# Kernel optimization log

Hardware: AMD Instinct MI355X
Metric: run time of the kernel (lower is better)

Reference implementation:

```python
import jax, jax.numpy as jnp
import numpy as np

N, E, H, ED = 10000, 160000, 512, 16
EPS = 1e-5
EDGE_SCALE = 0.1

def _ln(x, g, b):
    mu = jnp.mean(x, axis=-1, keepdims=True)
    var = jnp.mean(jnp.square(x - mu), axis=-1, keepdims=True)
    return (x - mu) * jax.lax.rsqrt(var + EPS) * g + b

def setup_inputs() -> dict:
    key = jax.random.key(0)
    ks = jax.random.split(key, 16)
    def w(k, i, o):
        return jax.random.normal(k, (i, o), jnp.float32) * (1.0 / np.sqrt(i))
    return {
        "h": jax.random.normal(ks[0], (N, H), jnp.float32),
        "edge_attr": jax.random.normal(ks[1], (E, ED), jnp.float32),
        "msg_w1": w(ks[2], H + ED, H), "msg_b1": jnp.zeros((H,), jnp.float32),
        "msg_w2": w(ks[3], H, H),      "msg_b2": jnp.zeros((H,), jnp.float32),
        "upd_w1": w(ks[4], 2 * H, H),  "upd_b1": jnp.zeros((H,), jnp.float32),
        "upd_w2": w(ks[5], H, H),      "upd_b2": jnp.zeros((H,), jnp.float32),
        "norm_g": jnp.ones((H,), jnp.float32), "norm_b": jnp.zeros((H,), jnp.float32),
        "em_w1": w(ks[6], 2 * H + ED, ED), "em_b1": jnp.zeros((ED,), jnp.float32),
        "em_w2": w(ks[7], ED, ED),         "em_b2": jnp.zeros((ED,), jnp.float32),
        "eg_w": w(ks[8], 2 * H + ED, 1),   "eg_b": jnp.zeros((1,), jnp.float32),
        "en_g": jnp.ones((ED,), jnp.float32), "en_b": jnp.zeros((ED,), jnp.float32),
        "edge_index": jax.random.randint(ks[9], (2, E), 0, N, jnp.int32),
    }

def reference(h, edge_attr, msg_w1, msg_b1, msg_w2, msg_b2,
              upd_w1, upd_b1, upd_w2, upd_b2, norm_g, norm_b,
              em_w1, em_b1, em_w2, em_b2, eg_w, eg_b, en_g, en_b,
              edge_index):
    src, dst = edge_index[0], edge_index[1]
    hs = h[src]                      # (E, H)
    hd = h[dst]                      # (E, H)
    # edge update with gating + scaled residual (eval: keep mask == 1)
    z = jnp.concatenate([hs, hd, edge_attr], axis=-1)   # (E, 2H+ED)
    gate = jax.nn.sigmoid(z @ eg_w + eg_b)               # (E, 1)
    delta = jax.nn.gelu(z @ em_w1 + em_b1, approximate=False) @ em_w2 + em_b2
    e_new = _ln(edge_attr + EDGE_SCALE * gate * delta, en_g, en_b)
    # message computation + scatter-add aggregation
    zm = jnp.concatenate([hs, e_new], axis=-1)           # (E, H+ED)
    m = jax.nn.gelu(zm @ msg_w1 + msg_b1, approximate=False) @ msg_w2 + msg_b2
    agg = jax.ops.segment_sum(m, dst, num_segments=h.shape[0])  # (N, H)
    # node update + residual + LayerNorm
    zu = jnp.concatenate([h, agg], axis=-1)              # (N, 2H)
    h2 = jax.nn.gelu(zu @ upd_w1 + upd_b1, approximate=False) @ upd_w2 + upd_b2
    h_out = _ln(h + h2, norm_g, norm_b)
    return (h_out, e_new)
```

## Files before the change

kernel.cpp:

```cpp
#include <hip/hip_runtime.h>

#define N_NODES 10000
#define N_EDGES 160000
#define HD 512
#define EDD 16

typedef unsigned short u16;
typedef __attribute__((ext_vector_type(8))) short bf16x8;
typedef __attribute__((ext_vector_type(4))) float f32x4;
typedef unsigned int u32;

__device__ __forceinline__ float bf2f(u16 u){
  unsigned int x = ((unsigned int)u) << 16;
  return __builtin_bit_cast(float, x);
}
__device__ __forceinline__ u16 f2bf(float f){
  unsigned int x = __builtin_bit_cast(unsigned int, f);
  unsigned int r = (x + 0x7fffu + ((x >> 16) & 1u)) >> 16;
  return (u16)r;
}
__device__ __forceinline__ float ldx(const void* p, long long i, int f32){
  return f32 ? ((const float*)p)[i] : bf2f(((const u16*)p)[i]);
}
__device__ __forceinline__ void stx(void* p, long long i, int f32, float v){
  if (f32) ((float*)p)[i] = v; else ((u16*)p)[i] = f2bf(v);
}
__device__ __forceinline__ float gelu_f(float x){
  float c = x * x;
  float a = x * (1.5957691216f + 0.0713548162f * c);
  float e = __expf(-a);
  return x * __builtin_amdgcn_rcpf(1.0f + e);
}
__device__ __forceinline__ f32x4 mfma16(bf16x8 a, bf16x8 b, f32x4 c){
  return __builtin_amdgcn_mfma_f32_16x16x32_bf16(a, b, c, 0, 0, 0);
}
__device__ __forceinline__ int swz8(int row, int slot){
  return (slot ^ ((row >> 1) & 3)) * 8;
}
__device__ __forceinline__ bf16x8 ld8(const void* p, long long i, int f32){
  if (!f32) return *(const bf16x8*)((const u16*)p + i);
  const float* q = (const float*)p + i;
  float4 a = *(const float4*)q, b = *(const float4*)(q + 4);
  u16 t[8] = { f2bf(a.x), f2bf(a.y), f2bf(a.z), f2bf(a.w),
               f2bf(b.x), f2bf(b.y), f2bf(b.z), f2bf(b.w) };
  return *(const bf16x8*)t;
}
__device__ __forceinline__ void stage8(const void* src, long long idx, int f32, u16* dst){
  bf16x8 v = ld8(src, idx, f32);
  *(bf16x8*)dst = v;
}

__device__ __forceinline__ int probe_rand(const void* p, int l){
  const u16* q = (const u16*)p;
  float mx = 0.f;
  #pragma unroll
  for (int i = 0; i < 4; ++i) mx = fmaxf(mx, fabsf(bf2f(q[l * 4 + i])));
  #pragma unroll
  for (int m = 1; m < 64; m <<= 1) mx = fmaxf(mx, __shfl_xor(mx, m, 64));
  return (mx > 1e3f) ? 1 : 0;
}
__global__ __launch_bounds__(64) void kprobe(
    const void* h, const void* ea, const void* mw1, const void* mw2,
    const void* uw1, const void* uw2, const void* ew1, const void* ew2,
    const void* egw, const void* ng, const void* eng, int* F)
{
  const int l = threadIdx.x;
  int f0 = probe_rand(h, l),   f1 = probe_rand(ea, l),  f2 = probe_rand(mw1, l);
  int f3 = probe_rand(mw2, l), f4 = probe_rand(uw1, l), f5 = probe_rand(uw2, l);
  int f6 = probe_rand(ew1, l), f7 = probe_rand(ew2, l), f8 = probe_rand(egw, l);
  if (l == 0){
    F[0] = f0; F[1] = f1; F[2] = f2; F[3] = f3; F[4] = f4; F[5] = f5;
    F[6] = f6; F[7] = f7; F[8] = f8;
    F[9]  = (((const u16*)ng)[0]  == 0) ? 1 : 0;
    F[10] = (((const u16*)eng)[0] == 0) ? 1 : 0;
    F[11] = f0;
  }
}

__global__ void kfill(u16* __restrict__ out, long long n, float val){
  long long i = (long long)blockIdx.x * 256 + threadIdx.x;
  if (i < n) out[i] = f2bf(val);
}

__global__ __launch_bounds__(256) void kprep(
    const void* __restrict__ h, const void* __restrict__ mw1,
    const void* __restrict__ mw2, const void* __restrict__ ew1,
    const void* __restrict__ egw, const int* __restrict__ F,
    u16* __restrict__ hB, u16* __restrict__ W1T, u16* __restrict__ W2T,
    u16* __restrict__ WceT)
{
  const int b = blockIdx.x, tid = threadIdx.x;
  if (b < 2500){
    const long long i = ((long long)b * 256 + tid) * 8;
    if (i < (long long)N_NODES * HD)
      *(bf16x8*)(hB + i) = ld8(h, i, F[0]);
  } else if (b < 3588){
    const int i = (b - 2500) * 256 + tid;
    const int n = i / 544, k = i - n * 544;
    u16 v = 0;
    if (k < 528) v = f2bf(ldx(mw1, (long long)k * 512 + n, F[2]));
    W1T[i] = v;
  } else if (b < 4612){
    const int i = (b - 3588) * 256 + tid;
    const int n = i >> 9, k = i & 511;
    W2T[i] = f2bf(ldx(mw2, (long long)k * 512 + n, F[3]));
  } else {
    const int i = (b - 4612) * 256 + tid;
    const int c = i >> 9, k = i & 511;
    float v = 0.f;
    if (c < 16)       v = ldx(ew1, (long long)k * 16 + c, F[6]);
    else if (c < 32)  v = ldx(ew1, (long long)(512 + k) * 16 + (c - 16), F[6]);
    else if (c == 32) v = ldx(egw, k, F[8]);
    else if (c == 33) v = ldx(egw, 512 + k, F[8]);
    WceT[i] = f2bf(v);
  }
}

__global__ __launch_bounds__(256) void kprep2(
    const void* __restrict__ uw1, const void* __restrict__ uw2,
    const int* __restrict__ F, u16* __restrict__ WU1T, u16* __restrict__ WU2T)
{
  const int b = blockIdx.x, tid = threadIdx.x;
  if (b < 2048){
    const int i = b * 256 + tid;
    const int n = i >> 10, k = i & 1023;
    WU1T[i] = f2bf(ldx(uw1, (long long)k * 512 + n, F[4]));
  } else {
    const int i = (b - 2048) * 256 + tid;
    const int n = i >> 9, k = i & 511;
    WU2T[i] = f2bf(ldx(uw2, (long long)k * 512 + n, F[5]));
  }
}

__global__ void kdeg(const int* __restrict__ dst, int* __restrict__ deg){
  int e = blockIdx.x * 256 + threadIdx.x;
  if (e < N_EDGES) atomicAdd(&deg[dst[e]], 1);
}

__global__ __launch_bounds__(256) void kscan(const int* __restrict__ deg,
                                             int* __restrict__ start){
  __shared__ int ls[256];
  const int t = threadIdx.x;
  const int base = t * 40;
  int s = 0;
  for (int i = 0; i < 40; ++i){ int idx = base + i; if (idx < N_NODES) s += deg[idx]; }
  ls[t] = s; __syncthreads();
  for (int off = 1; off < 256; off <<= 1){
    int v = (t >= off) ? ls[t - off] : 0;
    __syncthreads();
    ls[t] += v;
    __syncthreads();
  }
  int run = (t == 0) ? 0 : ls[t - 1];
  for (int i = 0; i < 40; ++i){
    int idx = base + i;
    if (idx < N_NODES){ start[idx] = run; run += deg[idx]; }
  }
}

__global__ void kscatter(const int* __restrict__ srcI, const int* __restrict__ dstI,
                         const int* __restrict__ start, int* __restrict__ cursor,
                         int* __restrict__ sSrc, int* __restrict__ sDst,
                         int* __restrict__ sIdx){
  int e = blockIdx.x * 256 + threadIdx.x;
  if (e < N_EDGES){
    int d = dstI[e];
    int p = start[d] + atomicAdd(&cursor[d], 1);
    sSrc[p] = srcI[e]; sDst[p] = d; sIdx[p] = e;
  }
}

__global__ __launch_bounds__(256, 4) void kpreP(
    const u16* __restrict__ hB, const u16* __restrict__ W1T,
    const void* __restrict__ msg_b1, const int* __restrict__ F,
    u16* __restrict__ P)
{
  __shared__ u16 As[128 * 32];
  __shared__ u16 Bs[64 * 32];
  const int tid = threadIdx.x;
  const int fw = F[2];
  const int row0 = blockIdx.x * 128, n0 = blockIdx.y * 64;
  f32x4 acc[2][4];
  f32x4 z4 = {0.f, 0.f, 0.f, 0.f};
  #pragma unroll
  for (int i = 0; i < 2; ++i)
    #pragma unroll
    for (int j = 0; j < 4; ++j) acc[i][j] = z4;
  const int w = tid >> 6, l = tid & 63;
  const int lm = l & 15, lk = l >> 4;
  const int nB = tid >> 2, kqB = tid & 3;
  for (int kt = 0; kt < 16; ++kt){
    const int kk = kt * 32;
    #pragma unroll
    for (int i = 0; i < 2; ++i){
      int t = tid + i * 256;
      int m = t >> 2, kq = t & 3;
      int gr = row0 + m; if (gr > N_NODES - 1) gr = N_NODES - 1;
      *(uint4*)&As[m * 32 + swz8(m, kq)] = *(const uint4*)(hB + (size_t)gr * HD + kk + kq * 8);
    }
    *(uint4*)&Bs[nB * 32 + swz8(nB, kqB)] =
        *(const uint4*)(W1T + (size_t)(n0 + nB) * 544 + kk + kqB * 8);
    __syncthreads();
    bf16x8 af[2], bfv[4];
    #pragma unroll
    for (int i = 0; i < 2; ++i){
      const int R = w * 32 + i * 16 + lm;
      af[i] = *(const bf16x8*)&As[R * 32 + swz8(R, lk)];
    }
    #pragma unroll
    for (int j = 0; j < 4; ++j){
      const int R = j * 16 + lm;
      bfv[j] = *(const bf16x8*)&Bs[R * 32 + swz8(R, lk)];
    }
    #pragma unroll
    for (int i = 0; i < 2; ++i)
      #pragma unroll
      for (int j = 0; j < 4; ++j)
        acc[i][j] = mfma16(af[i], bfv[j], acc[i][j]);
    __syncthreads();
  }
  #pragma unroll
  for (int j = 0; j < 4; ++j){
    const int col = n0 + j * 16 + lm;
    const float bias = ldx(msg_b1, col, fw);
    #pragma unroll
    for (int i = 0; i < 2; ++i){
      const int rb = row0 + w * 32 + i * 16 + lk * 4;
      #pragma unroll
      for (int r = 0; r < 4; ++r){
        int gr = rb + r;
        if (gr < N_NODES)
          P[(size_t)gr * HD + col] = f2bf(acc[i][j][r] + bias);
      }
    }
  }
}

__global__ __launch_bounds__(256) void kpreE(
    const u16* __restrict__ hB, const u16* __restrict__ WceT,
    u16* __restrict__ PE)
{
  __shared__ u16 As[128 * 32];
  __shared__ u16 Bs[48 * 32];
  const int tid = threadIdx.x;
  const int row0 = blockIdx.x * 128;
  f32x4 acc[2][3];
  f32x4 z4 = {0.f, 0.f, 0.f, 0.f};
  #pragma unroll
  for (int i = 0; i < 2; ++i)
    #pragma unroll
    for (int j = 0; j < 3; ++j) acc[i][j] = z4;
  const int w = tid >> 6, l = tid & 63;
  const int lm = l & 15, lk = l >> 4;
  for (int kt = 0; kt < 16; ++kt){
    const int kk = kt * 32;
    #pragma unroll
    for (int i = 0; i < 2; ++i){
      int t = tid + i * 256;
      int m = t >> 2, kq = t & 3;
      int gr = row0 + m; if (gr > N_NODES - 1) gr = N_NODES - 1;
      *(uint4*)&As[m * 32 + swz8(m, kq)] = *(const uint4*)(hB + (size_t)gr * HD + kk + kq * 8);
    }
    if (tid < 192){
      int c = tid >> 2, kq = tid & 3;
      *(uint4*)&Bs[c * 32 + swz8(c, kq)] =
          *(const uint4*)(WceT + (size_t)c * 512 + kk + kq * 8);
    }
    __syncthreads();
    bf16x8 af[2], bfv[3];
    #pragma unroll
    for (int i = 0; i < 2; ++i){
      const int R = w * 32 + i * 16 + lm;
      af[i] = *(const bf16x8*)&As[R * 32 + swz8(R, lk)];
    }
    #pragma unroll
    for (int j = 0; j < 3; ++j){
      const int R = j * 16 + lm;
      bfv[j] = *(const bf16x8*)&Bs[R * 32 + swz8(R, lk)];
    }
    #pragma unroll
    for (int i = 0; i < 2; ++i)
      #pragma unroll
      for (int j = 0; j < 3; ++j)
        acc[i][j] = mfma16(af[i], bfv[j], acc[i][j]);
    __syncthreads();
  }
  #pragma unroll
  for (int j = 0; j < 3; ++j){
    const int col = j * 16 + lm;
    #pragma unroll
    for (int i = 0; i < 2; ++i){
      const int rb = row0 + w * 32 + i * 16 + lk * 4;
      #pragma unroll
      for (int r = 0; r < 4; ++r){
        int gr = rb + r;
        if (gr < N_NODES)
          PE[(size_t)gr * 48 + col] = f2bf(acc[i][j][r]);
      }
    }
  }
}

__global__ __launch_bounds__(256) void kedge2(
    const void* __restrict__ ea, const u16* __restrict__ PE,
    const void* __restrict__ em_w1, const void* __restrict__ em_w2,
    const void* __restrict__ em_b1, const void* __restrict__ em_b2,
    const void* __restrict__ eg_w, const void* __restrict__ eg_b,
    const void* __restrict__ en_g, const void* __restrict__ en_b,
    const int* __restrict__ F,
    const int* __restrict__ srcI, const int* __restrict__ dstI,
    void* __restrict__ dout)
{
  __shared__ float wt[16][17];
  __shared__ float w2s[256];
  __shared__ float egt[16], b1e[16], b2s[16], gns[16], bns[16];
  __shared__ float egb_s;
  const int tid = threadIdx.x;
  const int fea = F[1], fem1 = F[6], fem2 = F[7], feg = F[8];
  const int fen = F[10], fo = F[11];
  { int k = tid >> 4, j = tid & 15;
    wt[k][j] = ldx(em_w1, (long long)(1024 + k) * 16 + j, fem1); }
  w2s[tid] = ldx(em_w2, tid, fem2);
  if (tid < 16){
    egt[tid] = ldx(eg_w, 1024 + tid, feg);
    b1e[tid] = ldx(em_b1, tid, fem1);
    b2s[tid] = ldx(em_b2, tid, fem2);
    gns[tid] = ldx(en_g, tid, fen);
    bns[tid] = ldx(en_b, tid, fen);
  }
  if (tid == 0) egb_s = ldx(eg_b, 0, feg);
  __syncthreads();

  const int e = blockIdx.x * 256 + tid;
  const int s = srcI[e], d = dstI[e];
  float earr[16];
  if (fea){
    const float4* q = (const float4*)((const float*)ea + (size_t)e * 16);
    float4 v0 = q[0], v1 = q[1], v2 = q[2], v3 = q[3];
    earr[0]=v0.x; earr[1]=v0.y; earr[2]=v0.z; earr[3]=v0.w;
    earr[4]=v1.x; earr[5]=v1.y; earr[6]=v1.z; earr[7]=v1.w;
    earr[8]=v2.x; earr[9]=v2.y; earr[10]=v2.z; earr[11]=v2.w;
    earr[12]=v3.x; earr[13]=v3.y; earr[14]=v3.z; earr[15]=v3.w;
  } else {
    const u16* q = (const u16*)ea + (size_t)e * 16;
    bf16x8 a = *(const bf16x8*)q, b = *(const bf16x8*)(q + 8);
    #pragma unroll
    for (int j = 0; j < 8; ++j){ earr[j] = bf2f((u16)a[j]); earr[8 + j] = bf2f((u16)b[j]); }
  }
  const u16* prs = PE + (size_t)s * 48;
  const u16* prd = PE + (size_t)d * 48;
  bf16x8 ps0 = *(const bf16x8*)prs,        ps1 = *(const bf16x8*)(prs + 8);
  bf16x8 pd0 = *(const bf16x8*)(prd + 16), pd1 = *(const bf16x8*)(prd + 24);
  const float gs = bf2f(prs[32]), gd = bf2f(prd[33]);
  float t[16];
  #pragma unroll
  for (int j = 0; j < 8; ++j){
    t[j]     = bf2f((u16)ps0[j]) + bf2f((u16)pd0[j]) + b1e[j];
    t[8 + j] = bf2f((u16)ps1[j]) + bf2f((u16)pd1[j]) + b1e[8 + j];
  }
  float gl = gs + gd + egb_s;
  #pragma unroll
  for (int k = 0; k < 16; ++k){
    const float ek = earr[k];
    gl += ek * egt[k];
    #pragma unroll
    for (int j = 0; j < 16; ++j) t[j] += ek * wt[k][j];
  }
  const float gate = __builtin_amdgcn_rcpf(1.0f + __expf(-gl));
  float gj[16];
  #pragma unroll
  for (int j = 0; j < 16; ++j) gj[j] = gelu_f(t[j]);
  float rv[16]; float s1 = 0.f, s2 = 0.f;
  #pragma unroll
  for (int j = 0; j < 16; ++j){
    float dlt = b2s[j];
    #pragma unroll
    for (int k = 0; k < 16; ++k) dlt += gj[k] * w2s[k * 16 + j];
    rv[j] = earr[j] + 0.1f * gate * dlt;
    s1 += rv[j]; s2 += rv[j] * rv[j];
  }
  const float mu  = s1 * (1.f / 16.f);
  const float var = s2 * (1.f / 16.f) - mu * mu;
  const float inv = rsqrtf(var + 1e-5f);
  if (fo){
    float* ob = (float*)dout + (size_t)N_NODES * HD + (size_t)e * 16;
    #pragma unroll
    for (int j = 0; j < 16; ++j) ob[j] = (rv[j] - mu) * inv * gns[j] + bns[j];
  } else {
    u16 tmp[16];
    #pragma unroll
    for (int j = 0; j < 16; ++j) tmp[j] = f2bf((rv[j] - mu) * inv * gns[j] + bns[j]);
    u16* ob = (u16*)dout + (size_t)N_NODES * HD + (size_t)e * 16;
    *(uint4*)ob = *(uint4*)&tmp[0];
    *(uint4*)(ob + 8) = *(uint4*)&tmp[8];
  }
}

__global__ __launch_bounds__(256, 4) void kmsg4(
    const u16* __restrict__ P, const void* __restrict__ dout,
    const u16* __restrict__ W1T, const int* __restrict__ F,
    const int* __restrict__ sSrc, const int* __restrict__ sDst,
    const int* __restrict__ sIdx,
    float* __restrict__ agg)
{
  __shared__ __align__(16) float SMEM[4352];
  u16*   As = (u16*)SMEM;
  u16*   Bs = (u16*)SMEM + 4096;
  float* Sf = SMEM;
  __shared__ int src_s[128];
  __shared__ int dst_s[128];
  const int tid = threadIdx.x;
  const int fo = F[11];
  const void* e_base = fo ? (const void*)((const float*)dout + (size_t)N_NODES * HD)
                          : (const void*)((const u16*)dout + (size_t)N_NODES * HD);
  const int row0 = blockIdx.x * 128, n0 = blockIdx.y * 128;
  if (tid < 128){
    src_s[tid] = sSrc[row0 + tid];
    dst_s[tid] = sDst[row0 + tid];
  }
  #pragma unroll
  for (int i = 0; i < 2; ++i){
    int t = tid + i * 256;
    int m = t >> 2, kq = t & 3;
    if (kq < 2){
      const long long ie = sIdx[row0 + m];
      stage8(e_base, ie * EDD + kq * 8, fo, &As[m * 32 + swz8(m, kq)]);
      *(uint4*)&Bs[m * 32 + swz8(m, kq)] =
          *(const uint4*)(W1T + (size_t)(n0 + m) * 544 + 512 + kq * 8);
    } else {
      uint4 z = {0,0,0,0};
      *(uint4*)&As[m * 32 + swz8(m, kq)] = z;
      *(uint4*)&Bs[m * 32 + swz8(m, kq)] = z;
    }
  }
  __syncthreads();
  const int w = tid >> 6, l = tid & 63;
  const int wr = w >> 1, wc = w & 1, lm = l & 15, lk = l >> 4;
  f32x4 acc[4][4];
  bf16x8 af[4], bfv[4];
  #pragma unroll
  for (int i = 0; i < 4; ++i){
    const int R = wr * 64 + i * 16 + lm;
    af[i] = *(const bf16x8*)&As[R * 32 + swz8(R, lk)];
  }
  #pragma unroll
  for (int j = 0; j < 4; ++j){
    const int R = wc * 64 + j * 16 + lm;
    bfv[j] = *(const bf16x8*)&Bs[R * 32 + swz8(R, lk)];
  }
  f32x4 z4 = {0.f, 0.f, 0.f, 0.f};
  #pragma unroll
  for (int i = 0; i < 4; ++i)
    #pragma unroll
    for (int j = 0; j < 4; ++j)
      acc[i][j] = mfma16(af[i], bfv[j], z4);
  u32 poff[4][4];
  #pragma unroll
  for (int i = 0; i < 4; ++i)
    #pragma unroll
    for (int r = 0; r < 4; ++r)
      poff[i][r] = (u32)src_s[wr * 64 + i * 16 + lk * 4 + r] * HD;
  const int cj = tid & 31, chunk = tid >> 5;
  const int rbase = chunk * 16;
  u32 aoff[16]; unsigned maskb = 0;
  {
    int dprev = dst_s[rbase];
    aoff[0] = (u32)dprev * HD;
    #pragma unroll
    for (int rr = 1; rr < 16; ++rr){
      const int dn = dst_s[rbase + rr];
      if (dn == dprev) maskb |= (1u << rr);
      aoff[rr] = (u32)dn * HD;
      dprev = dn;
    }
  }
  __syncthreads();
  const int sfb = wc * 16 + lm;
  #pragma unroll
  for (int j = 0; j < 4; ++j){
    const int col = n0 + wc * 64 + j * 16 + lm;
    #pragma unroll
    for (int i = 0; i < 4; ++i){
      #pragma unroll
      for (int r = 0; r < 4; ++r){
        const int row = wr * 64 + i * 16 + lk * 4 + r;
        const float pv = bf2f(P[poff[i][r] + col]);
        Sf[row * 34 + sfb] = gelu_f(acc[i][j][r] + pv);
      }
    }
    __syncthreads();
    const int acol = n0 + (cj >> 4) * 64 + j * 16 + (cj & 15);
    float run = Sf[rbase * 34 + cj];
    #pragma unroll
    for (int rr = 1; rr < 16; ++rr){
      const float v = Sf[(rbase + rr) * 34 + cj];
      if (maskb & (1u << rr)) run += v;
      else { atomicAdd(&agg[(size_t)aoff[rr - 1] + acol], run); run = v; }
    }
    atomicAdd(&agg[(size_t)aoff[15] + acol], run);
    __syncthreads();
  }
}

__global__ __launch_bounds__(256, 4) void kagg2(
    const float* __restrict__ S, const u16* __restrict__ W2T,
    const void* __restrict__ msg_b2, const int* __restrict__ F,
    const int* __restrict__ deg, u16* __restrict__ aggM)
{
  __shared__ u16 As[128 * 32];
  __shared__ u16 Bs[64 * 32];
  const int tid = threadIdx.x;
  const int fw = F[3];
  const int row0 = blockIdx.x * 128, n0 = blockIdx.y * 64;
  f32x4 acc[2][4];
  f32x4 z4 = {0.f, 0.f, 0.f, 0.f};
  #pragma unroll
  for (int i = 0; i < 2; ++i)
    #pragma unroll
    for (int j = 0; j < 4; ++j) acc[i][j] = z4;
  const int w = tid >> 6, l = tid & 63;
  const int lm = l & 15, lk = l >> 4;
  const int am = tid >> 1, ah = tid & 1;
  const int agr = row0 + am;
  const int nB = tid >> 2, kqB = tid & 3;
  for (int kt = 0; kt < 16; ++kt){
    const int kk = kt * 32;
    u16 tmp[16];
    if (agr < N_NODES){
      const float4* sp = (const float4*)(S + (size_t)agr * HD + kk + ah * 16);
      #pragma unroll
      for (int q = 0; q < 4; ++q){
        float4 v = sp[q];
        tmp[q*4+0] = f2bf(v.x); tmp[q*4+1] = f2bf(v.y);
        tmp[q*4+2] = f2bf(v.z); tmp[q*4+3] = f2bf(v.w);
      }
    } else {
      #pragma unroll
      for (int q = 0; q < 16; ++q) tmp[q] = 0;
    }
    *(uint4*)&As[am * 32 + swz8(am, ah * 2)]     = *(uint4*)&tmp[0];
    *(uint4*)&As[am * 32 + swz8(am, ah * 2 + 1)] = *(uint4*)&tmp[8];
    *(uint4*)&Bs[nB * 32 + swz8(nB, kqB)] =
        *(const uint4*)(W2T + (size_t)(n0 + nB) * 512 + kk + kqB * 8);
    __syncthreads();
    bf16x8 af[2], bfv[4];
    #pragma unroll
    for (int i = 0; i < 2; ++i){
      const int R = w * 32 + i * 16 + lm;
      af[i] = *(const bf16x8*)&As[R * 32 + swz8(R, lk)];
    }
    #pragma unroll
    for (int j = 0; j < 4; ++j){
      const int R = j * 16 + lm;
      bfv[j] = *(const bf16x8*)&Bs[R * 32 + swz8(R, lk)];
    }
    #pragma unroll
    for (int i = 0; i < 2; ++i)
      #pragma unroll
      for (int j = 0; j < 4; ++j)
        acc[i][j] = mfma16(af[i], bfv[j], acc[i][j]);
    __syncthreads();
  }
  #pragma unroll
  for (int j = 0; j < 4; ++j){
    const int col = n0 + j * 16 + lm;
    const float b2v = ldx(msg_b2, col, fw);
    #pragma unroll
    for (int i = 0; i < 2; ++i){
      const int rb = row0 + w * 32 + i * 16 + lk * 4;
      #pragma unroll
      for (int r = 0; r < 4; ++r){
        int gr = rb + r;
        if (gr < N_NODES)
          aggM[(size_t)gr * HD + col] = f2bf(acc[i][j][r] + (float)deg[gr] * b2v);
      }
    }
  }
}

__global__ __launch_bounds__(256, 4) void kupd1(
    const u16* __restrict__ hB, const u16* __restrict__ aggM,
    const u16* __restrict__ WU1T, const void* __restrict__ upd_b1,
    const int* __restrict__ F, u16* __restrict__ U)
{
  __shared__ u16 As[128 * 32];
  __shared__ u16 Bs[64 * 32];
  const int tid = threadIdx.x;
  const int fw = F[4];
  const int row0 = blockIdx.x * 128, n0 = blockIdx.y * 64;
  f32x4 acc[2][4];
  f32x4 z4 = {0.f, 0.f, 0.f, 0.f};
  #pragma unroll
  for (int i = 0; i < 2; ++i)
    #pragma unroll
    for (int j = 0; j < 4; ++j) acc[i][j] = z4;
  const int w = tid >> 6, l = tid & 63;
  const int lm = l & 15, lk = l >> 4;
  const int nB = tid >> 2, kqB = tid & 3;
  for (int kt = 0; kt < 32; ++kt){
    const int kk = kt * 32;
    #pragma unroll
    for (int i = 0; i < 2; ++i){
      int t = tid + i * 256;
      int m = t >> 2, kq = t & 3, c = kk + kq * 8;
      int gr = row0 + m; if (gr > N_NODES - 1) gr = N_NODES - 1;
      if (kk < 512) *(uint4*)&As[m * 32 + swz8(m, kq)] = *(const uint4*)(hB + (size_t)gr * HD + c);
      else          *(uint4*)&As[m * 32 + swz8(m, kq)] = *(const uint4*)(aggM + (size_t)gr * HD + (c - 512));
    }
    *(uint4*)&Bs[nB * 32 + swz8(nB, kqB)] =
        *(const uint4*)(WU1T + (size_t)(n0 + nB) * 1024 + kk + kqB * 8);
    __syncthreads();
    bf16x8 af[2], bfv[4];
    #pragma unroll
    for (int i = 0; i < 2; ++i){
      const int R = w * 32 + i * 16 + lm;
      af[i] = *(const bf16x8*)&As[R * 32 + swz8(R, lk)];
    }
    #pragma unroll
    for (int j = 0; j < 4; ++j){
      const int R = j * 16 + lm;
      bfv[j] = *(const bf16x8*)&Bs[R * 32 + swz8(R, lk)];
    }
    #pragma unroll
    for (int i = 0; i < 2; ++i)
      #pragma unroll
      for (int j = 0; j < 4; ++j)
        acc[i][j] = mfma16(af[i], bfv[j], acc[i][j]);
    __syncthreads();
  }
  #pragma unroll
  for (int j = 0; j < 4; ++j){
    const int col = n0 + j * 16 + lm;
    const float bias = ldx(upd_b1, col, fw);
    #pragma unroll
    for (int i = 0; i < 2; ++i){
      const int rb = row0 + w * 32 + i * 16 + lk * 4;
      #pragma unroll
      for (int r = 0; r < 4; ++r){
        int gr = rb + r;
        if (gr < N_NODES)
          U[(size_t)gr * HD + col] = f2bf(gelu_f(acc[i][j][r] + bias));
      }
    }
  }
}

__global__ __launch_bounds__(256, 4) void kupd2(
    const u16* __restrict__ U, const u16* __restrict__ WU2T,
    const void* __restrict__ upd_b2, const int* __restrict__ F,
    u16* __restrict__ h2b)
{
  __shared__ u16 As[128 * 32];
  __shared__ u16 Bs[64 * 32];
  const int tid = threadIdx.x;
  const int fw = F[5];
  const int row0 = blockIdx.x * 128, n0 = blockIdx.y * 64;
  f32x4 acc[2][4];
  f32x4 z4 = {0.f, 0.f, 0.f, 0.f};
  #pragma unroll
  for (int i = 0; i < 2; ++i)
    #pragma unroll
    for (int j = 0; j < 4; ++j) acc[i][j] = z4;
  const int w = tid >> 6, l = tid & 63;
  const int lm = l & 15, lk = l >> 4;
  const int nB = tid >> 2, kqB = tid & 3;
  for (int kt = 0; kt < 16; ++kt){
    const int kk = kt * 32;
    #pragma unroll
    for (int i = 0; i < 2; ++i){
      int t = tid + i * 256;
      int m = t >> 2, kq = t & 3;
      int gr = row0 + m; if (gr > N_NODES - 1) gr = N_NODES - 1;
      *(uint4*)&As[m * 32 + swz8(m, kq)] = *(const uint4*)(U + (size_t)gr * HD + kk + kq * 8);
    }
    *(uint4*)&Bs[nB * 32 + swz8(nB, kqB)] =
        *(const uint4*)(WU2T + (size_t)(n0 + nB) * 512 + kk + kqB * 8);
    __syncthreads();
    bf16x8 af[2], bfv[4];
    #pragma unroll
    for (int i = 0; i < 2; ++i){
      const int R = w * 32 + i * 16 + lm;
      af[i] = *(const bf16x8*)&As[R * 32 + swz8(R, lk)];
    }
    #pragma unroll
    for (int j = 0; j < 4; ++j){
      const int R = j * 16 + lm;
      bfv[j] = *(const bf16x8*)&Bs[R * 32 + swz8(R, lk)];
    }
    #pragma unroll
    for (int i = 0; i < 2; ++i)
      #pragma unroll
      for (int j = 0; j < 4; ++j)
        acc[i][j] = mfma16(af[i], bfv[j], acc[i][j]);
    __syncthreads();
  }
  #pragma unroll
  for (int j = 0; j < 4; ++j){
    const int col = n0 + j * 16 + lm;
    const float bias = ldx(upd_b2, col, fw);
    #pragma unroll
    for (int i = 0; i < 2; ++i){
      const int rb = row0 + w * 32 + i * 16 + lk * 4;
      #pragma unroll
      for (int r = 0; r < 4; ++r){
        int gr = rb + r;
        if (gr < N_NODES)
          h2b[(size_t)gr * HD + col] = f2bf(acc[i][j][r] + bias);
      }
    }
  }
}

__global__ __launch_bounds__(256) void kln(
    const void* __restrict__ h, const u16* __restrict__ h2b,
    const void* __restrict__ gg, const void* __restrict__ bbv,
    const int* __restrict__ F, void* __restrict__ dout)
{
  const int fh = F[0], fng = F[9], fo = F[11];
  const int w = threadIdx.x >> 6, l = threadIdx.x & 63;
  const int row = blockIdx.x * 4 + w;
  float x[8];
  #pragma unroll
  for (int j = 0; j < 8; ++j){
    const long long idx = (long long)row * HD + l * 8 + j;
    x[j] = ldx(h, idx, fh) + bf2f(h2b[idx]);
  }
  float s1 = 0.f, s2 = 0.f;
  #pragma unroll
  for (int j = 0; j < 8; ++j){ s1 += x[j]; s2 += x[j] * x[j]; }
  #pragma unroll
  for (int m = 1; m < 64; m <<= 1){ s1 += __shfl_xor(s1, m, 64); s2 += __shfl_xor(s2, m, 64); }
  const float mu  = s1 * (1.f / 512.f);
  const float var = s2 * (1.f / 512.f) - mu * mu;
  const float inv = rsqrtf(var + 1e-5f);
  #pragma unroll
  for (int j = 0; j < 8; ++j){
    const float gf = ldx(gg,  l * 8 + j, fng);
    const float bf = ldx(bbv, l * 8 + j, fng);
    stx(dout, (long long)row * HD + l * 8 + j, fo, (x[j] - mu) * inv * gf + bf);
  }
}

#define OFF_S     0u
#define OFF_DEG   20480000u
#define OFF_CUR   20520000u
#define OFF_F     20560000u
#define OFF_START 20560064u
#define OFF_AGGM  20600064u
#define OFF_W1T   30840064u
#define OFF_W2T   31397120u
#define OFF_WU1T  31921408u
#define OFF_WU2T  32969984u
#define OFF_WET   33494272u
#define OFF_SSRC  33528064u
#define OFF_SDST  34168064u
#define OFF_SIDX  34808064u
#define WS_NEEDED 35448064u

extern "C" void kernel_launch(void* const* d_in, const int* in_sizes, int n_in,
                              void* d_out, int out_size, void* d_ws, size_t ws_size,
                              hipStream_t stream)
{
  const void* h      = d_in[0];
  const void* ea     = d_in[1];
  const void* msg_w1 = d_in[2];
  const void* msg_b1 = d_in[3];
  const void* msg_w2 = d_in[4];
  const void* msg_b2 = d_in[5];
  const void* upd_w1 = d_in[6];
  const void* upd_b1 = d_in[7];
  const void* upd_w2 = d_in[8];
  const void* upd_b2 = d_in[9];
  const void* norm_g = d_in[10];
  const void* norm_b = d_in[11];
  const void* em_w1  = d_in[12];
  const void* em_b1  = d_in[13];
  const void* em_w2  = d_in[14];
  const void* em_b2  = d_in[15];
  const void* eg_w   = d_in[16];
  const void* eg_b   = d_in[17];
  const void* en_g   = d_in[18];
  const void* en_b   = d_in[19];
  const int* eidx    = (const int*)d_in[20];
  const int* srcI = eidx;
  const int* dstI = eidx + N_EDGES;

  float sent = 0.f;
  if (ws_size < (size_t)WS_NEEDED)            sent = 1000.f;
  else if (n_in != 21)                        sent = 2000.f;
  else if (in_sizes[0]  != N_NODES * HD)      sent = 3000.f;
  else if (in_sizes[20] != 2 * N_EDGES)       sent = 4000.f;
  else if (out_size != N_NODES*HD + N_EDGES*EDD) sent = 5000.f;
  if (sent != 0.f){
    kfill<<<(out_size + 255)/256, 256, 0, stream>>>((u16*)d_out, out_size, sent);
    return;
  }

  char* ws = (char*)d_ws;
  float* S     = (float*)(ws + OFF_S);
  u16*   U     = (u16*)(ws + OFF_S);
  int*   deg   = (int*)(ws + OFF_DEG);
  int*   cur   = (int*)(ws + OFF_CUR);
  int*   F     = (int*)(ws + OFF_F);
  int*   start = (int*)(ws + OFF_START);
  u16*   P     = (u16*)(ws + OFF_AGGM);
  u16*   aggM  = (u16*)(ws + OFF_AGGM);
  u16*   h2b   = (u16*)(ws + OFF_AGGM);
  u16*   W1T   = (u16*)(ws + OFF_W1T);
  u16*   W2T   = (u16*)(ws + OFF_W2T);
  u16*   PE    = (u16*)(ws + OFF_WU1T);
  u16*   WU1T  = (u16*)(ws + OFF_WU1T);
  u16*   WceT  = (u16*)(ws + OFF_WU2T);
  u16*   WU2T  = (u16*)(ws + OFF_WU2T);
  int*   sSrc  = (int*)(ws + OFF_SSRC);
  int*   sDst  = (int*)(ws + OFF_SDST);
  int*   sIdx  = (int*)(ws + OFF_SIDX);

  u16* hB = (u16*)d_out;

  hipMemsetAsync(S, 0, (size_t)OFF_F, stream);

  kprobe<<<1, 64, 0, stream>>>(h, ea, msg_w1, msg_w2, upd_w1, upd_w2,
                               em_w1, em_w2, eg_w, norm_g, en_g, F);

  kprep<<<4708, 256, 0, stream>>>(h, msg_w1, msg_w2, em_w1, eg_w, F,
                                  hB, W1T, W2T, WceT);

  kpreP<<<dim3(79, 8), 256, 0, stream>>>(hB, W1T, msg_b1, F, P);
  kpreE<<<79, 256, 0, stream>>>(hB, WceT, PE);

  kdeg<<<(N_EDGES + 255)/256, 256, 0, stream>>>(dstI, deg);
  kscan<<<1, 256, 0, stream>>>(deg, start);
  kscatter<<<(N_EDGES + 255)/256, 256, 0, stream>>>(srcI, dstI, start, cur,
                                                    sSrc, sDst, sIdx);

  kedge2<<<625, 256, 0, stream>>>(ea, PE, em_w1, em_w2, em_b1, em_b2, eg_w, eg_b,
                                  en_g, en_b, F, srcI, dstI, d_out);

  kprep2<<<3072, 256, 0, stream>>>(upd_w1, upd_w2, F, WU1T, WU2T);

  kmsg4<<<dim3(1250, 4), 256, 0, stream>>>(P, d_out, W1T, F,
                                           sSrc, sDst, sIdx, S);
  kagg2<<<dim3(79, 8), 256, 0, stream>>>(S, W2T, msg_b2, F, deg, aggM);
  kupd1<<<dim3(79, 8), 256, 0, stream>>>(hB, aggM, WU1T, upd_b1, F, U);
  kupd2<<<dim3(79, 8), 256, 0, stream>>>(U, WU2T, upd_b2, F, h2b);
  kln<<<2500, 256, 0, stream>>>(h, h2b, norm_g, norm_b, F, d_out);
}
```

Measured before the change: 416.0 us.

## Fold msg_w2 into upd_w1 and fuse aggregation GEMM into node update

Since agg = S·W2 + deg·b2 feeds linearly into the second half of upd_w1, the code precomputes the weight product W2·U1b and the bias vector b2·U1b. It then applies the product directly to the scattered sums S inside the node-update GEMM, which removes the separate kagg2 GEMM and its aggM round trip. It also replaces the element-wise weight transposes with 64x64 shared-memory tiled transposes, and merges the kpreP and kpreE kernels into one launch. The cost is a small weight-weight GEMM per call, plus extra bf16 rounding of the fused weight, which changes numerics slightly.

```diff
diff --git a/kernel.cpp b/kernel.cpp
--- a/kernel.cpp
+++ b/kernel.cpp
@@ -84,28 +84,38 @@
 
 __global__ __launch_bounds__(256) void kprep(
     const void* __restrict__ h, const void* __restrict__ mw1,
-    const void* __restrict__ mw2, const void* __restrict__ ew1,
-    const void* __restrict__ egw, const int* __restrict__ F,
-    u16* __restrict__ hB, u16* __restrict__ W1T, u16* __restrict__ W2T,
-    u16* __restrict__ WceT)
-{
+    const void* __restrict__ ew1, const void* __restrict__ egw,
+    const void* __restrict__ mb2, const void* __restrict__ uw1,
+    const int* __restrict__ F,
+    u16* __restrict__ hB, u16* __restrict__ W1T, u16* __restrict__ WceT,
+    float* __restrict__ bfused)
+{
+  __shared__ float tl[64][65];
   const int b = blockIdx.x, tid = threadIdx.x;
   if (b < 2500){
     const long long i = ((long long)b * 256 + tid) * 8;
     if (i < (long long)N_NODES * HD)
       *(bf16x8*)(hB + i) = ld8(h, i, F[0]);
-  } else if (b < 3588){
-    const int i = (b - 2500) * 256 + tid;
-    const int n = i / 544, k = i - n * 544;
-    u16 v = 0;
-    if (k < 528) v = f2bf(ldx(mw1, (long long)k * 512 + n, F[2]));
-    W1T[i] = v;
-  } else if (b < 4612){
-    const int i = (b - 3588) * 256 + tid;
-    const int n = i >> 9, k = i & 511;
-    W2T[i] = f2bf(ldx(mw2, (long long)k * 512 + n, F[3]));
-  } else {
-    const int i = (b - 4612) * 256 + tid;
+  } else if (b < 2572){
+    const int b2 = b - 2500;
+    const int kt0 = (b2 >> 3) * 64, nt0 = (b2 & 7) * 64;
+    const int ty = tid >> 6, tx = tid & 63;
+    const int fw = F[2];
+    #pragma unroll
+    for (int q = 0; q < 16; ++q){
+      const int r = ty * 16 + q;
+      const int sr = kt0 + r;
+      tl[r][tx] = (sr < 528) ? ldx(mw1, (long long)sr * 512 + nt0 + tx, fw) : 0.f;
+    }
+    __syncthreads();
+    #pragma unroll
+    for (int q = 0; q < 16; ++q){
+      const int r = ty * 16 + q;
+      const int k = kt0 + tx;
+      if (k < 544) W1T[(size_t)(nt0 + r) * 544 + k] = f2bf(tl[tx][r]);
+    }
+  } else if (b < 2668){
+    const int i = (b - 2572) * 256 + tid;
     const int c = i >> 9, k = i & 511;
     float v = 0.f;
     if (c < 16)       v = ldx(ew1, (long long)k * 16 + c, F[6]);
@@ -113,6 +123,16 @@
     else if (c == 32) v = ldx(egw, k, F[8]);
     else if (c == 33) v = ldx(egw, 512 + k, F[8]);
     WceT[i] = f2bf(v);
+  } else {
+    float* ls = &tl[0][0];
+    const int f3 = F[3], f4 = F[4];
+    for (int j = tid; j < 512; j += 256) ls[j] = ldx(mb2, j, f3);
+    __syncthreads();
+    const int n = (b - 2668) * 256 + tid;
+    float a = 0.f;
+    for (int j = 0; j < 512; ++j)
+      a += ls[j] * ldx(uw1, (long long)(512 + j) * 512 + n, f4);
+    bfused[n] = a;
   }
 }
 
@@ -120,15 +140,38 @@
     const void* __restrict__ uw1, const void* __restrict__ uw2,
     const int* __restrict__ F, u16* __restrict__ WU1T, u16* __restrict__ WU2T)
 {
+  __shared__ float tl[64][65];
   const int b = blockIdx.x, tid = threadIdx.x;
-  if (b < 2048){
-    const int i = b * 256 + tid;
-    const int n = i >> 10, k = i & 1023;
-    WU1T[i] = f2bf(ldx(uw1, (long long)k * 512 + n, F[4]));
+  const int ty = tid >> 6, tx = tid & 63;
+  if (b < 128){
+    const int kt0 = (b >> 3) * 64, nt0 = (b & 7) * 64;
+    const int fw = F[4];
+    #pragma unroll
+    for (int q = 0; q < 16; ++q){
+      const int r = ty * 16 + q;
+      tl[r][tx] = ldx(uw1, (long long)(kt0 + r) * 512 + nt0 + tx, fw);
+    }
+    __syncthreads();
+    #pragma unroll
+    for (int q = 0; q < 16; ++q){
+      const int r = ty * 16 + q;
+      WU1T[(size_t)(nt0 + r) * 1024 + kt0 + tx] = f2bf(tl[tx][r]);
+    }
   } else {
-    const int i = (b - 2048) * 256 + tid;
-    const int n = i >> 9, k = i & 511;
-    WU2T[i] = f2bf(ldx(uw2, (long long)k * 512 + n, F[5]));
+    const int b2 = b - 128;
+    const int kt0 = (b2 >> 3) * 64, nt0 = (b2 & 7) * 64;
+    const int fw = F[5];
+    #pragma unroll
+    for (int q = 0; q < 16; ++q){
+      const int r = ty * 16 + q;
+      tl[r][tx] = ldx(uw2, (long long)(kt0 + r) * 512 + nt0 + tx, fw);
+    }
+    __syncthreads();
+    #pragma unroll
+    for (int q = 0; q < 16; ++q){
+      const int r = ty * 16 + q;
+      WU2T[(size_t)(nt0 + r) * 512 + kt0 + tx] = f2bf(tl[tx][r]);
+    }
   }
 }
 
@@ -170,132 +213,124 @@
   }
 }
 
-__global__ __launch_bounds__(256, 4) void kpreP(
+__global__ __launch_bounds__(256, 4) void kprePE(
     const u16* __restrict__ hB, const u16* __restrict__ W1T,
-    const void* __restrict__ msg_b1, const int* __restrict__ F,
-    u16* __restrict__ P)
+    const void* __restrict__ msg_b1, const u16* __restrict__ WceT,
+    const int* __restrict__ F, u16* __restrict__ P, u16* __restrict__ PE)
 {
   __shared__ u16 As[128 * 32];
   __shared__ u16 Bs[64 * 32];
   const int tid = threadIdx.x;
-  const int fw = F[2];
-  const int row0 = blockIdx.x * 128, n0 = blockIdx.y * 64;
-  f32x4 acc[2][4];
-  f32x4 z4 = {0.f, 0.f, 0.f, 0.f};
-  #pragma unroll
-  for (int i = 0; i < 2; ++i)
-    #pragma unroll
-    for (int j = 0; j < 4; ++j) acc[i][j] = z4;
+  const int row0 = blockIdx.x * 128;
   const int w = tid >> 6, l = tid & 63;
   const int lm = l & 15, lk = l >> 4;
-  const int nB = tid >> 2, kqB = tid & 3;
-  for (int kt = 0; kt < 16; ++kt){
-    const int kk = kt * 32;
-    #pragma unroll
-    for (int i = 0; i < 2; ++i){
-      int t = tid + i * 256;
-      int m = t >> 2, kq = t & 3;
-      int gr = row0 + m; if (gr > N_NODES - 1) gr = N_NODES - 1;
-      *(uint4*)&As[m * 32 + swz8(m, kq)] = *(const uint4*)(hB + (size_t)gr * HD + kk + kq * 8);
-    }
-    *(uint4*)&Bs[nB * 32 + swz8(nB, kqB)] =
-        *(const uint4*)(W1T + (size_t)(n0 + nB) * 544 + kk + kqB * 8);
-    __syncthreads();
-    bf16x8 af[2], bfv[4];
-    #pragma unroll
-    for (int i = 0; i < 2; ++i){
-      const int R = w * 32 + i * 16 + lm;
-      af[i] = *(const bf16x8*)&As[R * 32 + swz8(R, lk)];
+  if (blockIdx.y < 8){
+    const int fw = F[2];
+    const int n0 = blockIdx.y * 64;
+    f32x4 acc[2][4];
+    f32x4 z4 = {0.f, 0.f, 0.f, 0.f};
+    #pragma unroll
+    for (int i = 0; i < 2; ++i)
+      #pragma unroll
+      for (int j = 0; j < 4; ++j) acc[i][j] = z4;
+    const int nB = tid >> 2, kqB = tid & 3;
+    for (int kt = 0; kt < 16; ++kt){
+      const int kk = kt * 32;
+      #pragma unroll
+      for (int i = 0; i < 2; ++i){
+        int t = tid + i * 256;
+        int m = t >> 2, kq = t & 3;
+        int gr = row0 + m; if (gr > N_NODES - 1) gr = N_NODES - 1;
+        *(uint4*)&As[m * 32 + swz8(m, kq)] = *(const uint4*)(hB + (size_t)gr * HD + kk + kq * 8);
+      }
+      *(uint4*)&Bs[nB * 32 + swz8(nB, kqB)] =
+          *(const uint4*)(W1T + (size_t)(n0 + nB) * 544 + kk + kqB * 8);
+      __syncthreads();
+      bf16x8 af[2], bfv[4];
+      #pragma unroll
+      for (int i = 0; i < 2; ++i){
+        const int R = w * 32 + i * 16 + lm;
+        af[i] = *(const bf16x8*)&As[R * 32 + swz8(R, lk)];
+      }
+      #pragma unroll
+      for (int j = 0; j < 4; ++j){
+        const int R = j * 16 + lm;
+        bfv[j] = *(const bf16x8*)&Bs[R * 32 + swz8(R, lk)];
+      }
+      #pragma unroll
+      for (int i = 0; i < 2; ++i)
+        #pragma unroll
+        for (int j = 0; j < 4; ++j)
+          acc[i][j] = mfma16(af[i], bfv[j], acc[i][j]);
+      __syncthreads();
     }
     #pragma unroll
     for (int j = 0; j < 4; ++j){
-      const int R = j * 16 + lm;
-      bfv[j] = *(const bf16x8*)&Bs[R * 32 + swz8(R, lk)];
-    }
+      const int col = n0 + j * 16 + lm;
+      const float bias = ldx(msg_b1, col, fw);
+      #pragma unroll
+      for (int i = 0; i < 2; ++i){
+        const int rb = row0 + w * 32 + i * 16 + lk * 4;
+        #pragma unroll
+        for (int r = 0; r < 4; ++r){
+          int gr = rb + r;
+          if (gr < N_NODES)
+            P[(size_t)gr * HD + col] = f2bf(acc[i][j][r] + bias);
+        }
+      }
+    }
+  } else {
+    f32x4 acc[2][3];
+    f32x4 z4 = {0.f, 0.f, 0.f, 0.f};
     #pragma unroll
     for (int i = 0; i < 2; ++i)
       #pragma unroll
-      for (int j = 0; j < 4; ++j)
-        acc[i][j] = mfma16(af[i], bfv[j], acc[i][j]);
-    __syncthreads();
-  }
-  #pragma unroll
-  for (int j = 0; j < 4; ++j){
-    const int col = n0 + j * 16 + lm;
-    const float bias = ldx(msg_b1, col, fw);
-    #pragma unroll
-    for (int i = 0; i < 2; ++i){
-      const int rb = row0 + w * 32 + i * 16 + lk * 4;
-      #pragma unroll
-      for (int r = 0; r < 4; ++r){
-        int gr = rb + r;
-        if (gr < N_NODES)
-          P[(size_t)gr * HD + col] = f2bf(acc[i][j][r] + bias);
-      }
-    }
-  }
-}
-
-__global__ __launch_bounds__(256) void kpreE(
-    const u16* __restrict__ hB, const u16* __restrict__ WceT,
-    u16* __restrict__ PE)
-{
-  __shared__ u16 As[128 * 32];
-  __shared__ u16 Bs[48 * 32];
-  const int tid = threadIdx.x;
-  const int row0 = blockIdx.x * 128;
-  f32x4 acc[2][3];
-  f32x4 z4 = {0.f, 0.f, 0.f, 0.f};
-  #pragma unroll
-  for (int i = 0; i < 2; ++i)
-    #pragma unroll
-    for (int j = 0; j < 3; ++j) acc[i][j] = z4;
-  const int w = tid >> 6, l = tid & 63;
-  const int lm = l & 15, lk = l >> 4;
-  for (int kt = 0; kt < 16; ++kt){
-    const int kk = kt * 32;
-    #pragma unroll
-    for (int i = 0; i < 2; ++i){
-      int t = tid + i * 256;
-      int m = t >> 2, kq = t & 3;
-      int gr = row0 + m; if (gr > N_NODES - 1) gr = N_NODES - 1;
-      *(uint4*)&As[m * 32 + swz8(m, kq)] = *(const uint4*)(hB + (size_t)gr * HD + kk + kq * 8);
-    }
-    if (tid < 192){
-      int c = tid >> 2, kq = tid & 3;
-      *(uint4*)&Bs[c * 32 + swz8(c, kq)] =
-          *(const uint4*)(WceT + (size_t)c * 512 + kk + kq * 8);
-    }
-    __syncthreads();
-    bf16x8 af[2], bfv[3];
-    #pragma unroll
-    for (int i = 0; i < 2; ++i){
-      const int R = w * 32 + i * 16 + lm;
-      af[i] = *(const bf16x8*)&As[R * 32 + swz8(R, lk)];
+      for (int j = 0; j < 3; ++j) acc[i][j] = z4;
+    for (int kt = 0; kt < 16; ++kt){
+      const int kk = kt * 32;
+      #pragma unroll
+      for (int i = 0; i < 2; ++i){
+        int t = tid + i * 256;
+        int m = t >> 2, kq = t & 3;
+        int gr = row0 + m; if (gr > N_NODES - 1) gr = N_NODES - 1;
+        *(uint4*)&As[m * 32 + swz8(m, kq)] = *(const uint4*)(hB + (size_t)gr * HD + kk + kq * 8);
+      }
+      if (tid < 192){
+        int c = tid >> 2, kq = tid & 3;
+        *(uint4*)&Bs[c * 32 + swz8(c, kq)] =
+            *(const uint4*)(WceT + (size_t)c * 512 + kk + kq * 8);
+      }
+      __syncthreads();
+      bf16x8 af[2], bfv[3];
+      #pragma unroll
+      for (int i = 0; i < 2; ++i){
+        const int R = w * 32 + i * 16 + lm;
+        af[i] = *(const bf16x8*)&As[R * 32 + swz8(R, lk)];
+      }
+      #pragma unroll
+      for (int j = 0; j < 3; ++j){
+        const int R = j * 16 + lm;
+        bfv[j] = *(const bf16x8*)&Bs[R * 32 + swz8(R, lk)];
+      }
+      #pragma unroll
+      for (int i = 0; i < 2; ++i)
+        #pragma unroll
+        for (int j = 0; j < 3; ++j)
+          acc[i][j] = mfma16(af[i], bfv[j], acc[i][j]);
+      __syncthreads();
     }
     #pragma unroll
     for (int j = 0; j < 3; ++j){
-      const int R = j * 16 + lm;
-      bfv[j] = *(const bf16x8*)&Bs[R * 32 + swz8(R, lk)];
-    }
-    #pragma unroll
-    for (int i = 0; i < 2; ++i)
-      #pragma unroll
-      for (int j = 0; j < 3; ++j)
-        acc[i][j] = mfma16(af[i], bfv[j], acc[i][j]);
-    __syncthreads();
-  }
-  #pragma unroll
-  for (int j = 0; j < 3; ++j){
-    const int col = j * 16 + lm;
-    #pragma unroll
-    for (int i = 0; i < 2; ++i){
-      const int rb = row0 + w * 32 + i * 16 + lk * 4;
-      #pragma unroll
-      for (int r = 0; r < 4; ++r){
-        int gr = rb + r;
-        if (gr < N_NODES)
-          PE[(size_t)gr * 48 + col] = f2bf(acc[i][j][r]);
+      const int col = j * 16 + lm;
+      #pragma unroll
+      for (int i = 0; i < 2; ++i){
+        const int rb = row0 + w * 32 + i * 16 + lk * 4;
+        #pragma unroll
+        for (int r = 0; r < 4; ++r){
+          int gr = rb + r;
+          if (gr < N_NODES)
+            PE[(size_t)gr * 48 + col] = f2bf(acc[i][j][r]);
+        }
       }
     }
   }
@@ -396,6 +431,67 @@
   }
 }
 
+__global__ __launch_bounds__(256, 4) void kWf(
+    const u16* __restrict__ WU1T, const void* __restrict__ mw2,
+    const int* __restrict__ F, u16* __restrict__ WfT)
+{
+  __shared__ u16 As[128 * 32];
+  __shared__ u16 Bs[64 * 32];
+  const int tid = threadIdx.x;
+  const int f3 = F[3];
+  const int row0 = blockIdx.x * 128, n0 = blockIdx.y * 64;
+  f32x4 acc[2][4];
+  f32x4 z4 = {0.f, 0.f, 0.f, 0.f};
+  #pragma unroll
+  for (int i = 0; i < 2; ++i)
+    #pragma unroll
+    for (int j = 0; j < 4; ++j) acc[i][j] = z4;
+  const int w = tid >> 6, l = tid & 63;
+  const int lm = l & 15, lk = l >> 4;
+  const int nB = tid >> 2, kqB = tid & 3;
+  for (int kt = 0; kt < 16; ++kt){
+    const int kk = kt * 32;
+    #pragma unroll
+    for (int i = 0; i < 2; ++i){
+      int t = tid + i * 256;
+      int m = t >> 2, kq = t & 3;
+      *(uint4*)&As[m * 32 + swz8(m, kq)] =
+          *(const uint4*)(WU1T + (size_t)(row0 + m) * 1024 + 512 + kk + kq * 8);
+    }
+    stage8(mw2, (long long)(n0 + nB) * 512 + kk + kqB * 8, f3,
+           &Bs[nB * 32 + swz8(nB, kqB)]);
+    __syncthreads();
+    bf16x8 af[2], bfv[4];
+    #pragma unroll
+    for (int i = 0; i < 2; ++i){
+      const int R = w * 32 + i * 16 + lm;
+      af[i] = *(const bf16x8*)&As[R * 32 + swz8(R, lk)];
+    }
+    #pragma unroll
+    for (int j = 0; j < 4; ++j){
+      const int R = j * 16 + lm;
+      bfv[j] = *(const bf16x8*)&Bs[R * 32 + swz8(R, lk)];
+    }
+    #pragma unroll
+    for (int i = 0; i < 2; ++i)
+      #pragma unroll
+      for (int j = 0; j < 4; ++j)
+        acc[i][j] = mfma16(af[i], bfv[j], acc[i][j]);
+    __syncthreads();
+  }
+  #pragma unroll
+  for (int j = 0; j < 4; ++j){
+    const int col = n0 + j * 16 + lm;
+    #pragma unroll
+    for (int i = 0; i < 2; ++i){
+      const int rb = row0 + w * 32 + i * 16 + lk * 4;
+      #pragma unroll
+      for (int r = 0; r < 4; ++r)
+        WfT[(size_t)(rb + r) * 512 + col] = f2bf(acc[i][j][r]);
+    }
+  }
+}
+
 __global__ __launch_bounds__(256, 4) void kmsg4(
     const u16* __restrict__ P, const void* __restrict__ dout,
     const u16* __restrict__ W1T, const int* __restrict__ F,
@@ -502,86 +598,12 @@
   }
 }
 
-__global__ __launch_bounds__(256, 4) void kagg2(
-    const float* __restrict__ S, const u16* __restrict__ W2T,
-    const void* __restrict__ msg_b2, const int* __restrict__ F,
-    const int* __restrict__ deg, u16* __restrict__ aggM)
-{
-  __shared__ u16 As[128 * 32];
-  __shared__ u16 Bs[64 * 32];
-  const int tid = threadIdx.x;
-  const int fw = F[3];
-  const int row0 = blockIdx.x * 128, n0 = blockIdx.y * 64;
-  f32x4 acc[2][4];
-  f32x4 z4 = {0.f, 0.f, 0.f, 0.f};
-  #pragma unroll
-  for (int i = 0; i < 2; ++i)
-    #pragma unroll
-    for (int j = 0; j < 4; ++j) acc[i][j] = z4;
-  const int w = tid >> 6, l = tid & 63;
-  const int lm = l & 15, lk = l >> 4;
-  const int am = tid >> 1, ah = tid & 1;
-  const int agr = row0 + am;
-  const int nB = tid >> 2, kqB = tid & 3;
-  for (int kt = 0; kt < 16; ++kt){
-    const int kk = kt * 32;
-    u16 tmp[16];
-    if (agr < N_NODES){
-      const float4* sp = (const float4*)(S + (size_t)agr * HD + kk + ah * 16);
-      #pragma unroll
-      for (int q = 0; q < 4; ++q){
-        float4 v = sp[q];
-        tmp[q*4+0] = f2bf(v.x); tmp[q*4+1] = f2bf(v.y);
-        tmp[q*4+2] = f2bf(v.z); tmp[q*4+3] = f2bf(v.w);
-      }
-    } else {
-      #pragma unroll
-      for (int q = 0; q < 16; ++q) tmp[q] = 0;
-    }
-    *(uint4*)&As[am * 32 + swz8(am, ah * 2)]     = *(uint4*)&tmp[0];
-    *(uint4*)&As[am * 32 + swz8(am, ah * 2 + 1)] = *(uint4*)&tmp[8];
-    *(uint4*)&Bs[nB * 32 + swz8(nB, kqB)] =
-        *(const uint4*)(W2T + (size_t)(n0 + nB) * 512 + kk + kqB * 8);
-    __syncthreads();
-    bf16x8 af[2], bfv[4];
-    #pragma unroll
-    for (int i = 0; i < 2; ++i){
-      const int R = w * 32 + i * 16 + lm;
-      af[i] = *(const bf16x8*)&As[R * 32 + swz8(R, lk)];
-    }
-    #pragma unroll
-    for (int j = 0; j < 4; ++j){
-      const int R = j * 16 + lm;
-      bfv[j] = *(const bf16x8*)&Bs[R * 32 + swz8(R, lk)];
-    }
-    #pragma unroll
-    for (int i = 0; i < 2; ++i)
-      #pragma unroll
-      for (int j = 0; j < 4; ++j)
-        acc[i][j] = mfma16(af[i], bfv[j], acc[i][j]);
-    __syncthreads();
-  }
-  #pragma unroll
-  for (int j = 0; j < 4; ++j){
-    const int col = n0 + j * 16 + lm;
-    const float b2v = ldx(msg_b2, col, fw);
-    #pragma unroll
-    for (int i = 0; i < 2; ++i){
-      const int rb = row0 + w * 32 + i * 16 + lk * 4;
-      #pragma unroll
-      for (int r = 0; r < 4; ++r){
-        int gr = rb + r;
-        if (gr < N_NODES)
-          aggM[(size_t)gr * HD + col] = f2bf(acc[i][j][r] + (float)deg[gr] * b2v);
-      }
-    }
-  }
-}
-
-__global__ __launch_bounds__(256, 4) void kupd1(
-    const u16* __restrict__ hB, const u16* __restrict__ aggM,
-    const u16* __restrict__ WU1T, const void* __restrict__ upd_b1,
-    const int* __restrict__ F, u16* __restrict__ U)
+__global__ __launch_bounds__(256, 4) void kupd1f(
+    const u16* __restrict__ hB, const float* __restrict__ S,
+    const u16* __restrict__ WU1T, const u16* __restrict__ WfT,
+    const void* __restrict__ upd_b1, const float* __restrict__ bfused,
+    const int* __restrict__ deg, const int* __restrict__ F,
+    u16* __restrict__ U)
 {
   __shared__ u16 As[128 * 32];
   __shared__ u16 Bs[64 * 32];
@@ -597,18 +619,40 @@
   const int w = tid >> 6, l = tid & 63;
   const int lm = l & 15, lk = l >> 4;
   const int nB = tid >> 2, kqB = tid & 3;
+  const int am = tid >> 1, ah = tid & 1;
+  const int agr = row0 + am;
   for (int kt = 0; kt < 32; ++kt){
     const int kk = kt * 32;
-    #pragma unroll
-    for (int i = 0; i < 2; ++i){
-      int t = tid + i * 256;
-      int m = t >> 2, kq = t & 3, c = kk + kq * 8;
-      int gr = row0 + m; if (gr > N_NODES - 1) gr = N_NODES - 1;
-      if (kk < 512) *(uint4*)&As[m * 32 + swz8(m, kq)] = *(const uint4*)(hB + (size_t)gr * HD + c);
-      else          *(uint4*)&As[m * 32 + swz8(m, kq)] = *(const uint4*)(aggM + (size_t)gr * HD + (c - 512));
-    }
-    *(uint4*)&Bs[nB * 32 + swz8(nB, kqB)] =
-        *(const uint4*)(WU1T + (size_t)(n0 + nB) * 1024 + kk + kqB * 8);
+    if (kk < 512){
+      #pragma unroll
+      for (int i = 0; i < 2; ++i){
+        int t = tid + i * 256;
+        int m = t >> 2, kq = t & 3;
+        int gr = row0 + m; if (gr > N_NODES - 1) gr = N_NODES - 1;
+        *(uint4*)&As[m * 32 + swz8(m, kq)] = *(const uint4*)(hB + (size_t)gr * HD + kk + kq * 8);
+      }
+      *(uint4*)&Bs[nB * 32 + swz8(nB, kqB)] =
+          *(const uint4*)(WU1T + (size_t)(n0 + nB) * 1024 + kk + kqB * 8);
+    } else {
+      const int ks = kk - 512;
+      u16 tmp[16];
+      if (agr < N_NODES){
+        const float4* sp = (const float4*)(S + (size_t)agr * HD + ks + ah * 16);
+        #pragma unroll
+        for (int q = 0; q < 4; ++q){
+          float4 v = sp[q];
+          tmp[q*4+0] = f2bf(v.x); tmp[q*4+1] = f2bf(v.y);
+          tmp[q*4+2] = f2bf(v.z); tmp[q*4+3] = f2bf(v.w);
+        }
+      } else {
+        #pragma unroll
+        for (int q = 0; q < 16; ++q) tmp[q] = 0;
+      }
+      *(uint4*)&As[am * 32 + swz8(am, ah * 2)]     = *(uint4*)&tmp[0];
+      *(uint4*)&As[am * 32 + swz8(am, ah * 2 + 1)] = *(uint4*)&tmp[8];
+      *(uint4*)&Bs[nB * 32 + swz8(nB, kqB)] =
+          *(const uint4*)(WfT + (size_t)(n0 + nB) * 512 + ks + kqB * 8);
+    }
     __syncthreads();
     bf16x8 af[2], bfv[4];
     #pragma unroll
@@ -632,6 +676,7 @@
   for (int j = 0; j < 4; ++j){
     const int col = n0 + j * 16 + lm;
     const float bias = ldx(upd_b1, col, fw);
+    const float bfv2 = bfused[col];
     #pragma unroll
     for (int i = 0; i < 2; ++i){
       const int rb = row0 + w * 32 + i * 16 + lk * 4;
@@ -639,7 +684,8 @@
       for (int r = 0; r < 4; ++r){
         int gr = rb + r;
         if (gr < N_NODES)
-          U[(size_t)gr * HD + col] = f2bf(gelu_f(acc[i][j][r] + bias));
+          U[(size_t)gr * HD + col] =
+              f2bf(gelu_f(acc[i][j][r] + bias + (float)deg[gr] * bfv2));
       }
     }
   }
@@ -797,24 +843,24 @@
   }
 
   char* ws = (char*)d_ws;
-  float* S     = (float*)(ws + OFF_S);
-  u16*   U     = (u16*)(ws + OFF_S);
-  int*   deg   = (int*)(ws + OFF_DEG);
-  int*   cur   = (int*)(ws + OFF_CUR);
-  int*   F     = (int*)(ws + OFF_F);
-  int*   start = (int*)(ws + OFF_START);
-  u16*   P     = (u16*)(ws + OFF_AGGM);
-  u16*   aggM  = (u16*)(ws + OFF_AGGM);
-  u16*   h2b   = (u16*)(ws + OFF_AGGM);
-  u16*   W1T   = (u16*)(ws + OFF_W1T);
-  u16*   W2T   = (u16*)(ws + OFF_W2T);
-  u16*   PE    = (u16*)(ws + OFF_WU1T);
-  u16*   WU1T  = (u16*)(ws + OFF_WU1T);
-  u16*   WceT  = (u16*)(ws + OFF_WU2T);
-  u16*   WU2T  = (u16*)(ws + OFF_WU2T);
-  int*   sSrc  = (int*)(ws + OFF_SSRC);
-  int*   sDst  = (int*)(ws + OFF_SDST);
-  int*   sIdx  = (int*)(ws + OFF_SIDX);
+  float* S      = (float*)(ws + OFF_S);
+  u16*   h2b    = (u16*)(ws + OFF_S);
+  int*   deg    = (int*)(ws + OFF_DEG);
+  int*   cur    = (int*)(ws + OFF_CUR);
+  int*   F      = (int*)(ws + OFF_F);
+  int*   start  = (int*)(ws + OFF_START);
+  u16*   P      = (u16*)(ws + OFF_AGGM);
+  u16*   U      = (u16*)(ws + OFF_AGGM);
+  u16*   W1T    = (u16*)(ws + OFF_W1T);
+  u16*   WfT    = (u16*)(ws + OFF_W2T);
+  u16*   PE     = (u16*)(ws + OFF_WU1T);
+  u16*   WU1T   = (u16*)(ws + OFF_WU1T);
+  u16*   WceT   = (u16*)(ws + OFF_WU2T);
+  u16*   WU2T   = (u16*)(ws + OFF_WU2T);
+  float* bfused = (float*)(ws + OFF_WET);
+  int*   sSrc   = (int*)(ws + OFF_SSRC);
+  int*   sDst   = (int*)(ws + OFF_SDST);
+  int*   sIdx   = (int*)(ws + OFF_SIDX);
 
   u16* hB = (u16*)d_out;
 
@@ -823,11 +869,10 @@
   kprobe<<<1, 64, 0, stream>>>(h, ea, msg_w1, msg_w2, upd_w1, upd_w2,
                                em_w1, em_w2, eg_w, norm_g, en_g, F);
 
-  kprep<<<4708, 256, 0, stream>>>(h, msg_w1, msg_w2, em_w1, eg_w, F,
-                                  hB, W1T, W2T, WceT);
-
-  kpreP<<<dim3(79, 8), 256, 0, stream>>>(hB, W1T, msg_b1, F, P);
-  kpreE<<<79, 256, 0, stream>>>(hB, WceT, PE);
+  kprep<<<2670, 256, 0, stream>>>(h, msg_w1, em_w1, eg_w, msg_b2, upd_w1, F,
+                                  hB, W1T, WceT, bfused);
+
+  kprePE<<<dim3(79, 9), 256, 0, stream>>>(hB, W1T, msg_b1, WceT, F, P, PE);
 
   kdeg<<<(N_EDGES + 255)/256, 256, 0, stream>>>(dstI, deg);
   kscan<<<1, 256, 0, stream>>>(deg, start);
@@ -837,12 +882,13 @@
   kedge2<<<625, 256, 0, stream>>>(ea, PE, em_w1, em_w2, em_b1, em_b2, eg_w, eg_b,
                                   en_g, en_b, F, srcI, dstI, d_out);
 
-  kprep2<<<3072, 256, 0, stream>>>(upd_w1, upd_w2, F, WU1T, WU2T);
+  kprep2<<<192, 256, 0, stream>>>(upd_w1, upd_w2, F, WU1T, WU2T);
+  kWf<<<dim3(4, 8), 256, 0, stream>>>(WU1T, msg_w2, F, WfT);
 
   kmsg4<<<dim3(1250, 4), 256, 0, stream>>>(P, d_out, W1T, F,
                                            sSrc, sDst, sIdx, S);
-  kagg2<<<dim3(79, 8), 256, 0, stream>>>(S, W2T, msg_b2, F, deg, aggM);
-  kupd1<<<dim3(79, 8), 256, 0, stream>>>(hB, aggM, WU1T, upd_b1, F, U);
+  kupd1f<<<dim3(79, 8), 256, 0, stream>>>(hB, S, WU1T, WfT, upd_b1, bfused,
+                                          deg, F, U);
   kupd2<<<dim3(79, 8), 256, 0, stream>>>(U, WU2T, upd_b2, F, h2b);
   kln<<<2500, 256, 0, stream>>>(h, h2b, norm_g, norm_b, F, d_out);
 }
```

Result: slower. 454.3 us (+9.2%).
